# Performance work log

Hardware: AMD Instinct MI355X
Metric: run time of the kernel (lower is better)

Reference implementation:

```python
import jax, jax.numpy as jnp
import numpy as np

B, C, N, K = 4, 192, 8192, 16
C_OUT = 192


def _gather_nodes(xs, idx):
    # xs: [B, C, N], idx: [B, N, K] -> [B, C, N, K]
    return jax.vmap(lambda xb, ib: xb[:, ib])(xs, idx)


def setup_inputs() -> dict:
    key = jax.random.key(0)
    k1, k2, k3 = jax.random.split(key, 3)
    x = jax.random.normal(k1, (B, C, N, 1), dtype=jnp.float32)
    x_0 = jnp.zeros((B, C, N, 1), dtype=jnp.float32)  # unused by forward, kept for interface
    edge_index = jax.random.randint(k2, (2, B, N, K), 0, N, dtype=jnp.int32)
    # 1x1 Conv2d(2C -> C_OUT) weight flattened to [C_OUT, 2C]
    W = jax.random.normal(k3, (C_OUT, 2 * C), dtype=jnp.float32) / np.sqrt(2 * C)
    b = jnp.zeros((C_OUT,), dtype=jnp.float32)
    return {"x": x, "x_0": x_0, "edge_index": edge_index, "W": W, "b": b}


def reference(x, x_0, edge_index, W, b):
    xs = x[..., 0]                       # [B, C, N]
    x_i = _gather_nodes(xs, edge_index[1])   # centers  [B, C, N, K]
    x_j = _gather_nodes(xs, edge_index[0])   # neighbors [B, C, N, K]
    rel = jnp.max(x_j - x_i, axis=-1)        # max-relative [B, C, N]
    y = jnp.concatenate([xs, rel], axis=1)   # [B, 2C, N]
    out = jnp.einsum('oc,bcn->bon', W, y) + b[None, :, None]  # 1x1 conv
    out = jax.nn.relu(out)
    return out[..., None]                # [B, C_OUT, N, 1]
```

## Files before the change

### kernel.cpp

```cpp
#include <hip/hip_runtime.h>

#define B_    4
#define C_    192
#define N_    8192
#define K_    16
#define O_    192
#define TWOC_ 384
#define YPAD  392

typedef __attribute__((ext_vector_type(8))) short short8;
typedef __attribute__((ext_vector_type(4))) short short4v;
typedef __attribute__((ext_vector_type(2))) unsigned int uint2v;
typedef __attribute__((ext_vector_type(4))) float floatx4;

static __device__ __forceinline__ float bf_lo(unsigned int u) {
    union { unsigned int i; float f; } v; v.i = u << 16; return v.f;
}
static __device__ __forceinline__ float bf_hi(unsigned int u) {
    union { unsigned int i; float f; } v; v.i = u & 0xffff0000u; return v.f;
}
static __device__ __forceinline__ unsigned short f2bf(float f) {
    union { float f; unsigned int i; } v; v.f = f;
    unsigned int x = v.i;
    return (unsigned short)((x + 0x7FFFu + ((x >> 16) & 1u)) >> 16);
}

__global__ __launch_bounds__(256) void k_prep(const float* __restrict__ x,
                                              const float* __restrict__ W,
                                              unsigned short* __restrict__ xt,
                                              unsigned short* __restrict__ Wb) {
    int bid = blockIdx.x;
    if (bid >= 6144) {
        int i = (bid - 6144) * 256 + threadIdx.x;
        if (i < O_ * TWOC_) Wb[i] = f2bf(W[i]);
        return;
    }
    __shared__ float tile[32][33];
    int xcd  = bid & 7;
    int b    = xcd >> 1;
    int half = xcd & 1;
    int slot = bid >> 3;
    int ct   = slot >> 7;
    int nt   = half * 128 + (slot & 127);
    int c0 = ct * 32, n0 = nt * 32;
    int tid = threadIdx.x;

    int cc  = tid >> 3;
    int nn4 = (tid & 7) * 4;
    const float* xp = x + ((size_t)b * C_ + c0 + cc) * N_ + n0 + nn4;
    float4 v = *(const float4*)xp;
    tile[nn4 + 0][cc] = v.x;
    tile[nn4 + 1][cc] = v.y;
    tile[nn4 + 2][cc] = v.z;
    tile[nn4 + 3][cc] = v.w;
    __syncthreads();

#pragma unroll
    for (int i = 0; i < 2; i++) {
        int id  = i * 256 + tid;
        int row = id >> 4;
        int ch2 = id & 15;
        float a = tile[row][ch2 * 2];
        float c = tile[row][ch2 * 2 + 1];
        unsigned int pack = (unsigned int)f2bf(a) | ((unsigned int)f2bf(c) << 16);
        *(unsigned int*)(xt + ((size_t)b * N_ + n0 + row) * C_ + c0 + ch2 * 2) = pack;
    }
}

__global__ __launch_bounds__(256, 4) void k_fused(const unsigned short* __restrict__ xt,
                                                  const int* __restrict__ eidx,
                                                  const unsigned short* __restrict__ Wb,
                                                  const float* __restrict__ bias,
                                                  float* __restrict__ out) {
    __shared__ unsigned short ytile[32][YPAD];
    __shared__ int sidx[32][33];

    int bid  = blockIdx.x;
    int xcd  = bid & 7;
    int b    = xcd >> 1;
    int slot = bid >> 3;
    int n0   = ((xcd & 1) * 128 + slot) * 32;

    int tid  = threadIdx.x;
    int wave = tid >> 6;
    int lane = tid & 63;

    const int* e0 = eidx + ((size_t)b * N_ + n0) * K_;
    const int* e1 = e0 + (size_t)B_ * N_ * K_;
#pragma unroll
    for (int i = 0; i < 2; i++) {
        int id = i * 256 + tid;
        int node = id >> 4, k = id & 15;
        sidx[node][k]      = e0[id];
        sidx[node][16 + k] = e1[id];
    }

    const unsigned short* xrow = xt + ((size_t)b * N_ + n0) * C_;
#pragma unroll
    for (int i = 0; i < 3; i++) {
        int id = i * 256 + tid;
        int row = id / 24, chunk = id % 24;
        short8 v = *(const short8*)(xrow + (size_t)row * C_ + chunk * 8);
        *(short8*)&ytile[row][chunk * 8] = v;
    }
    __syncthreads();

    {
        int g  = lane >> 4;
        int l4 = lane & 15;
        const unsigned short* xbase = xt + (size_t)b * N_ * C_;
#pragma unroll
        for (int bb = 0; bb < 2; bb++) {
            int node = wave * 8 + bb * 4 + g;
            uint2v bj[2][3], bi[2][3];
            {
                int jn = sidx[node][0], in = sidx[node][16];
                const unsigned short* pj = xbase + (size_t)jn * C_ + l4 * 4;
                const unsigned short* pi = xbase + (size_t)in * C_ + l4 * 4;
#pragma unroll
                for (int t = 0; t < 3; t++) {
                    bj[0][t] = *(const uint2v*)(pj + t * 64);
                    bi[0][t] = *(const uint2v*)(pi + t * 64);
                }
            }
            float m[3][4];
#pragma unroll
            for (int t = 0; t < 3; t++)
#pragma unroll
                for (int c = 0; c < 4; c++) m[t][c] = -INFINITY;

#pragma unroll
            for (int k = 0; k < K_; k++) {
                int cur = k & 1, nxt = cur ^ 1;
                if (k < K_ - 1) {
                    int jn = sidx[node][k + 1], in = sidx[node][16 + k + 1];
                    const unsigned short* pj = xbase + (size_t)jn * C_ + l4 * 4;
                    const unsigned short* pi = xbase + (size_t)in * C_ + l4 * 4;
#pragma unroll
                    for (int t = 0; t < 3; t++) {
                        bj[nxt][t] = *(const uint2v*)(pj + t * 64);
                        bi[nxt][t] = *(const uint2v*)(pi + t * 64);
                    }
                }
#pragma unroll
                for (int t = 0; t < 3; t++) {
                    uint2v vj = bj[cur][t], vi = bi[cur][t];
                    m[t][0] = fmaxf(m[t][0], bf_lo(vj.x) - bf_lo(vi.x));
                    m[t][1] = fmaxf(m[t][1], bf_hi(vj.x) - bf_hi(vi.x));
                    m[t][2] = fmaxf(m[t][2], bf_lo(vj.y) - bf_lo(vi.y));
                    m[t][3] = fmaxf(m[t][3], bf_hi(vj.y) - bf_hi(vi.y));
                }
            }
#pragma unroll
            for (int t = 0; t < 3; t++) {
                short4v s;
                s.x = (short)f2bf(m[t][0]);
                s.y = (short)f2bf(m[t][1]);
                s.z = (short)f2bf(m[t][2]);
                s.w = (short)f2bf(m[t][3]);
                *(short4v*)&ytile[node][C_ + t * 64 + l4 * 4] = s;
            }
        }
    }
    __syncthreads();

    int m16  = lane & 15;
    int quad = lane >> 4;
    const unsigned short* wbase = Wb + (size_t)(wave * 48 + m16) * TWOC_ + quad * 8;

    floatx4 acc[3][2];
#pragma unroll
    for (int i = 0; i < 3; i++)
#pragma unroll
        for (int j = 0; j < 2; j++) acc[i][j] = (floatx4){0.f, 0.f, 0.f, 0.f};

#pragma unroll
    for (int kt = 0; kt < 12; kt++) {
        short8 wf[3], yf[2];
#pragma unroll
        for (int i = 0; i < 3; i++)
            wf[i] = *(const short8*)(wbase + (size_t)(i * 16) * TWOC_ + kt * 32);
#pragma unroll
        for (int j = 0; j < 2; j++)
            yf[j] = *(const short8*)&ytile[j * 16 + m16][kt * 32 + quad * 8];
#pragma unroll
        for (int i = 0; i < 3; i++)
#pragma unroll
            for (int j = 0; j < 2; j++)
                acc[i][j] = __builtin_amdgcn_mfma_f32_16x16x32_bf16(wf[i], yf[j], acc[i][j], 0, 0, 0);
    }

#pragma unroll
    for (int i = 0; i < 3; i++) {
#pragma unroll
        for (int r = 0; r < 4; r++) {
            int o = wave * 48 + i * 16 + quad * 4 + r;
            float bv = bias[o];
#pragma unroll
            for (int j = 0; j < 2; j++) {
                int n = n0 + j * 16 + m16;
                out[((size_t)b * O_ + o) * N_ + n] = fmaxf(acc[i][j][r] + bv, 0.f);
            }
        }
    }
}

extern "C" void kernel_launch(void* const* d_in, const int* in_sizes, int n_in,
                              void* d_out, int out_size, void* d_ws, size_t ws_size,
                              hipStream_t stream) {
    const float* x    = (const float*)d_in[0];
    const int*   eidx = (const int*)d_in[2];
    const float* W    = (const float*)d_in[3];
    const float* bias = (const float*)d_in[4];
    float*       out  = (float*)d_out;

    unsigned short* Wb = (unsigned short*)d_ws;
    unsigned short* xt = (unsigned short*)((char*)d_ws + 147456);

    k_prep<<<dim3(6144 + 288), dim3(256), 0, stream>>>(x, W, xt, Wb);
    k_fused<<<dim3(1024), dim3(256), 0, stream>>>(xt, eidx, Wb, bias, out);
}
```

Baseline: 141.6 us.

## Deepen gather prefetch to two stages and vectorize index loads

The gather loop now keeps a three-slot register ring so that loads for neighbor k+2 are issued while k is reduced, replacing the previous one-ahead double buffer. All 32 indices for a node are read up front from LDS with int4 loads, and the LDS row is padded to 36 so those vector reads stay aligned. The prep kernel is also split into separate W-conversion and transpose launches, which adds a kernel launch. The deeper ring raises register pressure, which could reduce occupancy under the 4-blocks-per-CU launch bound.

```diff
diff --git a/kernel.cpp b/kernel.cpp
--- a/kernel.cpp
+++ b/kernel.cpp
@@ -25,17 +25,16 @@
     return (unsigned short)((x + 0x7FFFu + ((x >> 16) & 1u)) >> 16);
 }
 
-__global__ __launch_bounds__(256) void k_prep(const float* __restrict__ x,
-                                              const float* __restrict__ W,
-                                              unsigned short* __restrict__ xt,
-                                              unsigned short* __restrict__ Wb) {
-    int bid = blockIdx.x;
-    if (bid >= 6144) {
-        int i = (bid - 6144) * 256 + threadIdx.x;
-        if (i < O_ * TWOC_) Wb[i] = f2bf(W[i]);
-        return;
-    }
+__global__ __launch_bounds__(256) void k_convert_w(const float* __restrict__ W,
+                                                   unsigned short* __restrict__ Wb) {
+    int i = blockIdx.x * 256 + threadIdx.x;
+    if (i < O_ * TWOC_) Wb[i] = f2bf(W[i]);
+}
+
+__global__ __launch_bounds__(256) void k_transpose(const float* __restrict__ x,
+                                                   unsigned short* __restrict__ xt) {
     __shared__ float tile[32][33];
+    int bid  = blockIdx.x;
     int xcd  = bid & 7;
     int b    = xcd >> 1;
     int half = xcd & 1;
@@ -73,7 +72,7 @@
                                                   const float* __restrict__ bias,
                                                   float* __restrict__ out) {
     __shared__ unsigned short ytile[32][YPAD];
-    __shared__ int sidx[32][33];
+    __shared__ int sidx[32][36];
 
     int bid  = blockIdx.x;
     int xcd  = bid & 7;
@@ -109,42 +108,54 @@
         int g  = lane >> 4;
         int l4 = lane & 15;
         const unsigned short* xbase = xt + (size_t)b * N_ * C_;
+
+#define GLD(BJ, BI, JN, IN)                                                 \
+        {                                                                   \
+            const unsigned short* pj = xbase + (size_t)(JN) * C_ + l4 * 4;  \
+            const unsigned short* pi = xbase + (size_t)(IN) * C_ + l4 * 4;  \
+            BJ[0] = *(const uint2v*)(pj);                                   \
+            BI[0] = *(const uint2v*)(pi);                                   \
+            BJ[1] = *(const uint2v*)(pj + 64);                              \
+            BI[1] = *(const uint2v*)(pi + 64);                              \
+            BJ[2] = *(const uint2v*)(pj + 128);                             \
+            BI[2] = *(const uint2v*)(pi + 128);                             \
+        }
+
 #pragma unroll
         for (int bb = 0; bb < 2; bb++) {
             int node = wave * 8 + bb * 4 + g;
-            uint2v bj[2][3], bi[2][3];
-            {
-                int jn = sidx[node][0], in = sidx[node][16];
-                const unsigned short* pj = xbase + (size_t)jn * C_ + l4 * 4;
-                const unsigned short* pi = xbase + (size_t)in * C_ + l4 * 4;
+
+            int ji[K_], ii[K_];
+#pragma unroll
+            for (int t = 0; t < 4; t++) {
+                int4 a = *(const int4*)&sidx[node][t * 4];
+                int4 c = *(const int4*)&sidx[node][16 + t * 4];
+                ji[t * 4 + 0] = a.x; ji[t * 4 + 1] = a.y;
+                ji[t * 4 + 2] = a.z; ji[t * 4 + 3] = a.w;
+                ii[t * 4 + 0] = c.x; ii[t * 4 + 1] = c.y;
+                ii[t * 4 + 2] = c.z; ii[t * 4 + 3] = c.w;
+            }
+
+            uint2v bj[3][3], bi[3][3];
+            GLD(bj[0], bi[0], ji[0], ii[0]);
+            GLD(bj[1], bi[1], ji[1], ii[1]);
+
+            float m[3][4];
+#pragma unroll
+            for (int t = 0; t < 3; t++)
+#pragma unroll
+                for (int c = 0; c < 4; c++) m[t][c] = -INFINITY;
+
+#pragma unroll
+            for (int k = 0; k < K_; k++) {
+                int cb = k % 3;
+                if (k + 2 < K_) {
+                    int pb = (k + 2) % 3;
+                    GLD(bj[pb], bi[pb], ji[k + 2], ii[k + 2]);
+                }
 #pragma unroll
                 for (int t = 0; t < 3; t++) {
-                    bj[0][t] = *(const uint2v*)(pj + t * 64);
-                    bi[0][t] = *(const uint2v*)(pi + t * 64);
-                }
-            }
-            float m[3][4];
-#pragma unroll
-            for (int t = 0; t < 3; t++)
-#pragma unroll
-                for (int c = 0; c < 4; c++) m[t][c] = -INFINITY;
-
-#pragma unroll
-            for (int k = 0; k < K_; k++) {
-                int cur = k & 1, nxt = cur ^ 1;
-                if (k < K_ - 1) {
-                    int jn = sidx[node][k + 1], in = sidx[node][16 + k + 1];
-                    const unsigned short* pj = xbase + (size_t)jn * C_ + l4 * 4;
-                    const unsigned short* pi = xbase + (size_t)in * C_ + l4 * 4;
-#pragma unroll
-                    for (int t = 0; t < 3; t++) {
-                        bj[nxt][t] = *(const uint2v*)(pj + t * 64);
-                        bi[nxt][t] = *(const uint2v*)(pi + t * 64);
-                    }
-                }
-#pragma unroll
-                for (int t = 0; t < 3; t++) {
-                    uint2v vj = bj[cur][t], vi = bi[cur][t];
+                    uint2v vj = bj[cb][t], vi = bi[cb][t];
                     m[t][0] = fmaxf(m[t][0], bf_lo(vj.x) - bf_lo(vi.x));
                     m[t][1] = fmaxf(m[t][1], bf_hi(vj.x) - bf_hi(vi.x));
                     m[t][2] = fmaxf(m[t][2], bf_lo(vj.y) - bf_lo(vi.y));
@@ -161,6 +172,7 @@
                 *(short4v*)&ytile[node][C_ + t * 64 + l4 * 4] = s;
             }
         }
+#undef GLD
     }
     __syncthreads();
 
@@ -217,6 +229,7 @@
     unsigned short* Wb = (unsigned short*)d_ws;
     unsigned short* xt = (unsigned short*)((char*)d_ws + 147456);
 
-    k_prep<<<dim3(6144 + 288), dim3(256), 0, stream>>>(x, W, xt, Wb);
+    k_convert_w<<<dim3(288), dim3(256), 0, stream>>>(W, Wb);
+    k_transpose<<<dim3(6144), dim3(256), 0, stream>>>(x, xt);
     k_fused<<<dim3(1024), dim3(256), 0, stream>>>(xt, eidx, Wb, bias, out);
 }
```

Measured after the change: 143.8 us. About the same (+1.6%).

## Halve nodes per block, double grid, deepen gather prefetch to three buffers

Applied to the files above, without the earlier changes.

The fused gather+GEMM kernel now handles 16 nodes per block instead of 32, launches 2048 blocks, and raises launch bounds to 8 blocks per SM. Each wave processes one node group instead of two sequential ones. The gather loop uses a triple-buffered prefetch of two neighbours ahead to hide more load latency. The aim is more waves in flight during the latency-bound gather. In exchange, weight fragments are reloaded twice as often per output column, and each MFMA tile now covers only 16 columns.

```diff
diff --git a/kernel.cpp b/kernel.cpp
--- a/kernel.cpp
+++ b/kernel.cpp
@@ -7,6 +7,7 @@
 #define O_    192
 #define TWOC_ 384
 #define YPAD  392
+#define NB_   16
 
 typedef __attribute__((ext_vector_type(8))) short short8;
 typedef __attribute__((ext_vector_type(4))) short short4v;
@@ -67,99 +68,103 @@
     }
 }
 
-__global__ __launch_bounds__(256, 4) void k_fused(const unsigned short* __restrict__ xt,
+__global__ __launch_bounds__(256, 8) void k_fused(const unsigned short* __restrict__ xt,
                                                   const int* __restrict__ eidx,
                                                   const unsigned short* __restrict__ Wb,
                                                   const float* __restrict__ bias,
                                                   float* __restrict__ out) {
-    __shared__ unsigned short ytile[32][YPAD];
-    __shared__ int sidx[32][33];
+    __shared__ unsigned short ytile[NB_][YPAD];
+    __shared__ int sidx[NB_][36];
 
     int bid  = blockIdx.x;
     int xcd  = bid & 7;
     int b    = xcd >> 1;
     int slot = bid >> 3;
-    int n0   = ((xcd & 1) * 128 + slot) * 32;
+    int n0   = ((xcd & 1) * 256 + slot) * NB_;
 
     int tid  = threadIdx.x;
     int wave = tid >> 6;
     int lane = tid & 63;
 
-    const int* e0 = eidx + ((size_t)b * N_ + n0) * K_;
-    const int* e1 = e0 + (size_t)B_ * N_ * K_;
-#pragma unroll
-    for (int i = 0; i < 2; i++) {
-        int id = i * 256 + tid;
-        int node = id >> 4, k = id & 15;
-        sidx[node][k]      = e0[id];
-        sidx[node][16 + k] = e1[id];
-    }
-
-    const unsigned short* xrow = xt + ((size_t)b * N_ + n0) * C_;
-#pragma unroll
-    for (int i = 0; i < 3; i++) {
-        int id = i * 256 + tid;
-        int row = id / 24, chunk = id % 24;
-        short8 v = *(const short8*)(xrow + (size_t)row * C_ + chunk * 8);
-        *(short8*)&ytile[row][chunk * 8] = v;
+    {
+        const int* e0 = eidx + ((size_t)b * N_ + n0) * K_;
+        const int* e1 = e0 + (size_t)B_ * N_ * K_;
+        int node = tid >> 4, k = tid & 15;
+        sidx[node][k]      = e0[tid];
+        sidx[node][16 + k] = e1[tid];
+    }
+
+    {
+        const unsigned short* xrow = xt + ((size_t)b * N_ + n0) * C_;
+        int id = tid;
+        {
+            int row = id / 24, chunk = id % 24;
+            short8 v = *(const short8*)(xrow + (size_t)row * C_ + chunk * 8);
+            *(short8*)&ytile[row][chunk * 8] = v;
+        }
+        id = 256 + tid;
+        if (id < 384) {
+            int row = id / 24, chunk = id % 24;
+            short8 v = *(const short8*)(xrow + (size_t)row * C_ + chunk * 8);
+            *(short8*)&ytile[row][chunk * 8] = v;
+        }
     }
     __syncthreads();
 
     {
         int g  = lane >> 4;
         int l4 = lane & 15;
+        int node = wave * 4 + g;
         const unsigned short* xbase = xt + (size_t)b * N_ * C_;
-#pragma unroll
-        for (int bb = 0; bb < 2; bb++) {
-            int node = wave * 8 + bb * 4 + g;
-            uint2v bj[2][3], bi[2][3];
-            {
-                int jn = sidx[node][0], in = sidx[node][16];
-                const unsigned short* pj = xbase + (size_t)jn * C_ + l4 * 4;
-                const unsigned short* pi = xbase + (size_t)in * C_ + l4 * 4;
-#pragma unroll
-                for (int t = 0; t < 3; t++) {
-                    bj[0][t] = *(const uint2v*)(pj + t * 64);
-                    bi[0][t] = *(const uint2v*)(pi + t * 64);
-                }
+
+#define GLD(BUF, JN, IN)                                                    \
+        {                                                                   \
+            const unsigned short* pj = xbase + (size_t)(JN) * C_ + l4 * 4;  \
+            const unsigned short* pi = xbase + (size_t)(IN) * C_ + l4 * 4;  \
+            bj[BUF][0] = *(const uint2v*)(pj);                              \
+            bi[BUF][0] = *(const uint2v*)(pi);                              \
+            bj[BUF][1] = *(const uint2v*)(pj + 64);                         \
+            bi[BUF][1] = *(const uint2v*)(pi + 64);                         \
+            bj[BUF][2] = *(const uint2v*)(pj + 128);                        \
+            bi[BUF][2] = *(const uint2v*)(pi + 128);                        \
+        }
+
+        uint2v bj[3][3], bi[3][3];
+        GLD(0, sidx[node][0], sidx[node][16]);
+        GLD(1, sidx[node][1], sidx[node][17]);
+
+        float m[3][4];
+#pragma unroll
+        for (int t = 0; t < 3; t++)
+#pragma unroll
+            for (int c = 0; c < 4; c++) m[t][c] = -INFINITY;
+
+#pragma unroll
+        for (int k = 0; k < K_; k++) {
+            int cb = k % 3;
+            if (k + 2 < K_) {
+                int pb = (k + 2) % 3;
+                GLD(pb, sidx[node][k + 2], sidx[node][16 + k + 2]);
             }
-            float m[3][4];
-#pragma unroll
-            for (int t = 0; t < 3; t++)
-#pragma unroll
-                for (int c = 0; c < 4; c++) m[t][c] = -INFINITY;
-
-#pragma unroll
-            for (int k = 0; k < K_; k++) {
-                int cur = k & 1, nxt = cur ^ 1;
-                if (k < K_ - 1) {
-                    int jn = sidx[node][k + 1], in = sidx[node][16 + k + 1];
-                    const unsigned short* pj = xbase + (size_t)jn * C_ + l4 * 4;
-                    const unsigned short* pi = xbase + (size_t)in * C_ + l4 * 4;
-#pragma unroll
-                    for (int t = 0; t < 3; t++) {
-                        bj[nxt][t] = *(const uint2v*)(pj + t * 64);
-                        bi[nxt][t] = *(const uint2v*)(pi + t * 64);
-                    }
-                }
-#pragma unroll
-                for (int t = 0; t < 3; t++) {
-                    uint2v vj = bj[cur][t], vi = bi[cur][t];
-                    m[t][0] = fmaxf(m[t][0], bf_lo(vj.x) - bf_lo(vi.x));
-                    m[t][1] = fmaxf(m[t][1], bf_hi(vj.x) - bf_hi(vi.x));
-                    m[t][2] = fmaxf(m[t][2], bf_lo(vj.y) - bf_lo(vi.y));
-                    m[t][3] = fmaxf(m[t][3], bf_hi(vj.y) - bf_hi(vi.y));
-                }
+#pragma unroll
+            for (int t = 0; t < 3; t++) {
+                uint2v vj = bj[cb][t], vi = bi[cb][t];
+                m[t][0] = fmaxf(m[t][0], bf_lo(vj.x) - bf_lo(vi.x));
+                m[t][1] = fmaxf(m[t][1], bf_hi(vj.x) - bf_hi(vi.x));
+                m[t][2] = fmaxf(m[t][2], bf_lo(vj.y) - bf_lo(vi.y));
+                m[t][3] = fmaxf(m[t][3], bf_hi(vj.y) - bf_hi(vi.y));
             }
-#pragma unroll
-            for (int t = 0; t < 3; t++) {
-                short4v s;
-                s.x = (short)f2bf(m[t][0]);
-                s.y = (short)f2bf(m[t][1]);
-                s.z = (short)f2bf(m[t][2]);
-                s.w = (short)f2bf(m[t][3]);
-                *(short4v*)&ytile[node][C_ + t * 64 + l4 * 4] = s;
-            }
+        }
+#undef GLD
+
+#pragma unroll
+        for (int t = 0; t < 3; t++) {
+            short4v s;
+            s.x = (short)f2bf(m[t][0]);
+            s.y = (short)f2bf(m[t][1]);
+            s.z = (short)f2bf(m[t][2]);
+            s.w = (short)f2bf(m[t][3]);
+            *(short4v*)&ytile[node][C_ + t * 64 + l4 * 4] = s;
         }
     }
     __syncthreads();
@@ -168,26 +173,18 @@
     int quad = lane >> 4;
     const unsigned short* wbase = Wb + (size_t)(wave * 48 + m16) * TWOC_ + quad * 8;
 
-    floatx4 acc[3][2];
-#pragma unroll
-    for (int i = 0; i < 3; i++)
-#pragma unroll
-        for (int j = 0; j < 2; j++) acc[i][j] = (floatx4){0.f, 0.f, 0.f, 0.f};
+    floatx4 acc[3];
+#pragma unroll
+    for (int i = 0; i < 3; i++) acc[i] = (floatx4){0.f, 0.f, 0.f, 0.f};
 
 #pragma unroll
     for (int kt = 0; kt < 12; kt++) {
-        short8 wf[3], yf[2];
-#pragma unroll
-        for (int i = 0; i < 3; i++)
-            wf[i] = *(const short8*)(wbase + (size_t)(i * 16) * TWOC_ + kt * 32);
-#pragma unroll
-        for (int j = 0; j < 2; j++)
-            yf[j] = *(const short8*)&ytile[j * 16 + m16][kt * 32 + quad * 8];
-#pragma unroll
-        for (int i = 0; i < 3; i++)
-#pragma unroll
-            for (int j = 0; j < 2; j++)
-                acc[i][j] = __builtin_amdgcn_mfma_f32_16x16x32_bf16(wf[i], yf[j], acc[i][j], 0, 0, 0);
+        short8 yf = *(const short8*)&ytile[m16][kt * 32 + quad * 8];
+#pragma unroll
+        for (int i = 0; i < 3; i++) {
+            short8 wf = *(const short8*)(wbase + (size_t)(i * 16) * TWOC_ + kt * 32);
+            acc[i] = __builtin_amdgcn_mfma_f32_16x16x32_bf16(wf, yf, acc[i], 0, 0, 0);
+        }
     }
 
 #pragma unroll
@@ -195,12 +192,7 @@
 #pragma unroll
         for (int r = 0; r < 4; r++) {
             int o = wave * 48 + i * 16 + quad * 4 + r;
-            float bv = bias[o];
-#pragma unroll
-            for (int j = 0; j < 2; j++) {
-                int n = n0 + j * 16 + m16;
-                out[((size_t)b * O_ + o) * N_ + n] = fmaxf(acc[i][j][r] + bv, 0.f);
-            }
+            out[((size_t)b * O_ + o) * N_ + n0 + m16] = fmaxf(acc[i][r] + bias[o], 0.f);
         }
     }
 }
@@ -218,5 +210,5 @@
     unsigned short* xt = (unsigned short*)((char*)d_ws + 147456);
 
     k_prep<<<dim3(6144 + 288), dim3(256), 0, stream>>>(x, W, xt, Wb);
-    k_fused<<<dim3(1024), dim3(256), 0, stream>>>(xt, eidx, Wb, bias, out);
-}
+    k_fused<<<dim3(2048), dim3(256), 0, stream>>>(xt, eidx, Wb, bias, out);
+}
```

Result: slower. 223.4 us (+57.8%).
